# Performance work log

Hardware: AMD Instinct MI355X
Metric: run time of the kernel (lower is better)

Reference implementation:

```python
import jax, jax.numpy as jnp
import numpy as np

H = 128   # hidden_dim
M = 8     # mix_dim
N = 20000 # num_nodes
E = 320000

def gelu(x):
    return jax.nn.gelu(x, approximate=False)  # torch F.gelu default is exact erf

def setup_inputs() -> dict:
    key = jax.random.key(0)
    k1, k2, k3, k4 = jax.random.split(key, 4)
    X = jax.random.normal(k1, (N, H), dtype=jnp.float32)
    edge_index = jax.random.randint(k2, (2, E), 0, N, dtype=jnp.int64)
    # Linear weights, torch layout: y = x @ W.T
    W_A = jax.random.normal(k3, (H, H), dtype=jnp.float32) / np.sqrt(H)
    W_B = jax.random.normal(k4, (M, H), dtype=jnp.float32) / np.sqrt(H)
    return {"X": X, "edge_index": edge_index, "W_A": W_A, "W_B": W_B, "num_nodes": N}

def reference(X, edge_index, W_A, W_B, num_nodes):
    src, dst = edge_index[0], edge_index[1]
    X_src = X[src]                                   # (E, h) gather
    # compute_W_tar: W_B(gelu(W_A(X_src))), input_activation=False
    W_tar_edge = gelu(X_src @ W_A.T) @ W_B.T         # (E, m)
    # per-edge outer product, scatter_add over dst
    cross = jnp.einsum('eh,em->ehm', X_src, W_tar_edge)          # (E, h, m)
    agg = jax.ops.segment_sum(cross, dst, num_segments=num_nodes) # (N, h, m)
    agg = gelu(agg)
    # gather agg back to edges, contract over mix dim
    out_edge = jnp.einsum('ehm,em->eh', agg[dst], W_tar_edge)     # (E, h)
    # scatter_mean over dst
    ones = jnp.ones((dst.shape[0],), dtype=X.dtype)
    count = jax.ops.segment_sum(ones, dst, num_segments=num_nodes)
    out_sum = jax.ops.segment_sum(out_edge, dst, num_segments=num_nodes)
    out = out_sum / jnp.maximum(count, 1.0)[:, None]
    return out
```

## Files before the change

### kernel.cpp

```cpp
#include <hip/hip_runtime.h>
#include <hip/hip_bf16.h>


#define H 128
#define MDIM 8
#define CAP 64

typedef float v2f __attribute__((ext_vector_type(2)));

__device__ __forceinline__ float gelu_f(float x) {
    float x2 = x * x;
    float u  = x * (0.7978845608f + 0.0356774081f * x2);
    float u2 = u * u;
    float num = u * (945.0f + u2 * (105.0f + u2));
    float den = 945.0f + u2 * (420.0f + 15.0f * u2);
    float t = num * __builtin_amdgcn_rcpf(den);
    t = fminf(fmaxf(t, -1.0f), 1.0f);
    return 0.5f * (x + x * t);
}

__device__ __forceinline__ v2f gelu2(v2f x) {
    v2f x2 = x * x;
    v2f u  = x * (0.7978845608f + 0.0356774081f * x2);
    v2f u2 = u * u;
    v2f num = u * (945.0f + u2 * (105.0f + u2));
    v2f den = 945.0f + u2 * (420.0f + 15.0f * u2);
    v2f t;
    t.x = num.x * __builtin_amdgcn_rcpf(den.x);
    t.y = num.y * __builtin_amdgcn_rcpf(den.y);
    t.x = fminf(fmaxf(t.x, -1.0f), 1.0f);
    t.y = fminf(fmaxf(t.y, -1.0f), 1.0f);
    return 0.5f * (x + x * t);
}

__global__ __launch_bounds__(128) void k_prep_fill(const float* __restrict__ X,
                                                   const float* __restrict__ WA,
                                                   const float* __restrict__ WB,
                                                   const int* __restrict__ ei,
                                                   float* __restrict__ T,
                                                   int* __restrict__ cnt,
                                                   int* __restrict__ bucket,
                                                   int N, int E) {
    __shared__ float Xs[32][68];
    __shared__ float Ws[128][68];
    __shared__ float WBs[8][132];
    const int t  = threadIdx.x;
    const int n0 = blockIdx.x * 32;
    const int tn = t >> 4;
    const int tj = t & 15;

    #pragma unroll
    for (int i = 0; i < 2; ++i) {
        int idx = t + 128 * i;
        int r = idx >> 5, c4 = idx & 31;
        *(float4*)&WBs[r][c4 * 4] = *(const float4*)(WB + (size_t)r * H + c4 * 4);
    }

    float acc[4][8] = {};

    for (int kh = 0; kh < 2; ++kh) {
        __syncthreads();
        const int kb = kh * 64;
        #pragma unroll
        for (int i = 0; i < 4; ++i) {
            int idx = t + 128 * i;
            int r = idx >> 4, c4 = idx & 15;
            *(float4*)&Xs[r][c4 * 4] =
                *(const float4*)(X + (size_t)(n0 + r) * H + kb + c4 * 4);
        }
        #pragma unroll
        for (int i = 0; i < 16; ++i) {
            int idx = t + 128 * i;
            int r = idx >> 4, c4 = idx & 15;
            *(float4*)&Ws[r][c4 * 4] =
                *(const float4*)(WA + (size_t)r * H + kb + c4 * 4);
        }
        __syncthreads();

        #pragma unroll 1
        for (int k = 0; k < 64; k += 4) {
            float4 xv[4], bv[8];
            #pragma unroll
            for (int nn = 0; nn < 4; ++nn)
                xv[nn] = *(const float4*)&Xs[4 * tn + nn][k];
            #pragma unroll
            for (int jj = 0; jj < 8; ++jj)
                bv[jj] = *(const float4*)&Ws[tj + 16 * jj][k];
            #pragma unroll
            for (int nn = 0; nn < 4; ++nn)
                #pragma unroll
                for (int jj = 0; jj < 8; ++jj)
                    acc[nn][jj] += xv[nn].x * bv[jj].x + xv[nn].y * bv[jj].y +
                                   xv[nn].z * bv[jj].z + xv[nn].w * bv[jj].w;
        }
    }

    __syncthreads();
    float (*Hs)[132] = (float(*)[132])Ws;
    #pragma unroll
    for (int nn = 0; nn < 4; ++nn)
        #pragma unroll
        for (int jj = 0; jj < 8; ++jj)
            Hs[4 * tn + nn][tj + 16 * jj] = gelu_f(acc[nn][jj]);
    __syncthreads();

    #pragma unroll
    for (int i = 0; i < 2; ++i) {
        int q = t + 128 * i;
        int n = q >> 3, m = q & 7;
        float s = 0.f;
        #pragma unroll 4
        for (int kk = 0; kk < 32; ++kk) {
            float4 h = *(const float4*)&Hs[n][kk * 4];
            float4 w = *(const float4*)&WBs[m][kk * 4];
            s += h.x * w.x + h.y * w.y + h.z * w.z + h.w * w.w;
        }
        T[(size_t)(n0 + n) * MDIM + m] = s;
    }

    {
        const int stride = gridDim.x * 128;
        for (int e = blockIdx.x * 128 + t; e < E; e += stride) {
            int s  = ei[e];
            int dd = ei[E + e];
            int p  = atomicAdd(&cnt[dd], 1);
            if (p < CAP) bucket[dd * CAP + p] = s;
        }
    }
}

__device__ __forceinline__ void fma8v(v2f* acc, v2f xv, float4 ta, float4 tb) {
    acc[0] += xv * ta.x;
    acc[1] += xv * ta.y;
    acc[2] += xv * ta.z;
    acc[3] += xv * ta.w;
    acc[4] += xv * tb.x;
    acc[5] += xv * tb.y;
    acc[6] += xv * tb.z;
    acc[7] += xv * tb.w;
}

__global__ __launch_bounds__(256) void k_main(const float* __restrict__ X,
                                              const float* __restrict__ T,
                                              const int* __restrict__ cnt,
                                              const int* __restrict__ bucket,
                                              float* __restrict__ out, int N) {
    __shared__ __attribute__((aligned(16))) int srcs[4][CAP];
    __shared__ float Tl[4][CAP][MDIM];
    const int w    = threadIdx.x >> 6;
    const int lane = threadIdx.x & 63;
    const int d    = blockIdx.x * 4 + w;
    if (d >= N) return;

    const int c  = cnt[d];
    const int cc = (c < CAP) ? c : CAP;

    if (lane < cc) {
        int s = bucket[d * CAP + lane];
        srcs[w][lane] = s;
        const float4* t4 = (const float4*)(T + (size_t)s * MDIM);
        *(float4*)&Tl[w][lane][0] = t4[0];
        *(float4*)&Tl[w][lane][4] = t4[1];
    }

    float sp = 0.f;
    {
        const int m = lane & 7, g = lane >> 3;
        for (int j = g; j < cc; j += 8) sp += Tl[w][j][m];
        sp += __shfl_xor(sp, 8);
        sp += __shfl_xor(sp, 16);
        sp += __shfl_xor(sp, 32);
    }
    float S[MDIM];
    #pragma unroll
    for (int m = 0; m < MDIM; ++m) S[m] = __shfl(sp, m);

    v2f acc[MDIM] = {};
    const float* Xl = X + 2 * lane;

    int j = 0;
    for (; j + 8 <= cc; j += 8) {
        int4 sa = *(const int4*)&srcs[w][j];
        int4 sb = *(const int4*)&srcs[w][j + 4];
        v2f x0 = *(const v2f*)(Xl + (size_t)sa.x * H);
        v2f x1 = *(const v2f*)(Xl + (size_t)sa.y * H);
        v2f x2 = *(const v2f*)(Xl + (size_t)sa.z * H);
        v2f x3 = *(const v2f*)(Xl + (size_t)sa.w * H);
        v2f x4 = *(const v2f*)(Xl + (size_t)sb.x * H);
        v2f x5 = *(const v2f*)(Xl + (size_t)sb.y * H);
        v2f x6 = *(const v2f*)(Xl + (size_t)sb.z * H);
        v2f x7 = *(const v2f*)(Xl + (size_t)sb.w * H);
        #pragma unroll
        for (int q = 0; q < 8; ++q) {
            float4 ta = *(const float4*)&Tl[w][j + q][0];
            float4 tb = *(const float4*)&Tl[w][j + q][4];
            v2f xv = (q == 0) ? x0 : (q == 1) ? x1 : (q == 2) ? x2 : (q == 3) ? x3
                   : (q == 4) ? x4 : (q == 5) ? x5 : (q == 6) ? x6 : x7;
            fma8v(acc, xv, ta, tb);
        }
    }
    for (; j + 4 <= cc; j += 4) {
        int4 s4 = *(const int4*)&srcs[w][j];
        v2f x0 = *(const v2f*)(Xl + (size_t)s4.x * H);
        v2f x1 = *(const v2f*)(Xl + (size_t)s4.y * H);
        v2f x2 = *(const v2f*)(Xl + (size_t)s4.z * H);
        v2f x3 = *(const v2f*)(Xl + (size_t)s4.w * H);
        fma8v(acc, x0, *(const float4*)&Tl[w][j + 0][0], *(const float4*)&Tl[w][j + 0][4]);
        fma8v(acc, x1, *(const float4*)&Tl[w][j + 1][0], *(const float4*)&Tl[w][j + 1][4]);
        fma8v(acc, x2, *(const float4*)&Tl[w][j + 2][0], *(const float4*)&Tl[w][j + 2][4]);
        fma8v(acc, x3, *(const float4*)&Tl[w][j + 3][0], *(const float4*)&Tl[w][j + 3][4]);
    }
    for (; j < cc; ++j) {
        int s = srcs[w][j];
        v2f xv = *(const v2f*)(Xl + (size_t)s * H);
        float4 ta = *(const float4*)&Tl[w][j][0];
        float4 tb = *(const float4*)&Tl[w][j][4];
        fma8v(acc, xv, ta, tb);
    }

    v2f r = {0.f, 0.f};
    if (c > 0) {
        float inv = __builtin_amdgcn_rcpf((float)c);
        #pragma unroll
        for (int m = 0; m < MDIM; ++m) r += gelu2(acc[m]) * S[m];
        r.x *= inv;
        r.y *= inv;
    }
    *(v2f*)(out + (size_t)d * H + 2 * lane) = r;
}

extern "C" void kernel_launch(void* const* d_in, const int* in_sizes, int n_in,
                              void* d_out, int out_size, void* d_ws, size_t ws_size,
                              hipStream_t stream) {
    const float* X  = (const float*)d_in[0];
    const int*   ei = (const int*)d_in[1];
    const float* WA = (const float*)d_in[2];
    const float* WB = (const float*)d_in[3];
    float* out = (float*)d_out;

    const int N = in_sizes[0] / H;
    const int E = in_sizes[1] / 2;

    char* wp = (char*)d_ws;
    float* T    = (float*)wp;  wp += (size_t)N * MDIM * sizeof(float);
    int*   cnt  = (int*)wp;    wp += (size_t)((N + 3) & ~3) * sizeof(int);
    int*   bucket = (int*)wp;

    hipMemsetAsync(cnt, 0, (size_t)N * sizeof(int), stream);
    k_prep_fill<<<dim3(N / 32), dim3(128), 0, stream>>>(
        X, WA, WB, ei, T, cnt, bucket, N, E);
    k_main<<<dim3((N + 3) / 4), dim3(256), 0, stream>>>(X, T, cnt, bucket, out, N);
}
```

Baseline: 126.3 us.

## Compute X@W_A^T with split-bf16 MFMA and prefetch bucket sources unconditionally

```diff
diff --git a/kernel.cpp b/kernel.cpp
--- a/kernel.cpp
+++ b/kernel.cpp
@@ -1,5 +1,4 @@
 #include <hip/hip_runtime.h>
-#include <hip/hip_bf16.h>
 
 
 #define H 128
@@ -7,6 +6,11 @@
 #define CAP 64
 
 typedef float v2f __attribute__((ext_vector_type(2)));
+typedef float f32x4 __attribute__((ext_vector_type(4)));
+typedef short bf16x8 __attribute__((ext_vector_type(8)));
+typedef unsigned int uint2v __attribute__((ext_vector_type(2)));
+
+union FragCvt { unsigned int u[4]; bf16x8 s8; };
 
 __device__ __forceinline__ float gelu_f(float x) {
     float x2 = x * x;
@@ -41,67 +45,102 @@
                                                    int* __restrict__ cnt,
                                                    int* __restrict__ bucket,
                                                    int N, int E) {
-    __shared__ float Xs[32][68];
-    __shared__ float Ws[128][68];
-    __shared__ float WBs[8][132];
-    const int t  = threadIdx.x;
-    const int n0 = blockIdx.x * 32;
-    const int tn = t >> 4;
-    const int tj = t & 15;
-
+    __shared__ __align__(16) char lds[65536];
+    char* WAh = lds;
+    char* WAl = lds + 32768;
+
+    const int t    = threadIdx.x;
+    const int n0   = blockIdx.x * 32;
+    const int w    = t >> 6;
+    const int lane = t & 63;
+    const int tj   = lane & 15;
+    const int tc   = lane >> 4;
+
+    const float* xp = X + (size_t)(n0 + w * 16 + tj) * H + tc * 8;
+    f32x4 xr[8];
+    #pragma unroll
+    for (int ks = 0; ks < 4; ++ks) {
+        xr[2 * ks]     = *(const f32x4*)(xp + ks * 32);
+        xr[2 * ks + 1] = *(const f32x4*)(xp + ks * 32 + 4);
+    }
+
+    #pragma unroll
+    for (int i = 0; i < 32; ++i) {
+        int idx = t + 128 * i;
+        int r = idx >> 5, c4 = idx & 31;
+        f32x4 v = *(const f32x4*)(WA + (size_t)r * H + c4 * 4);
+        unsigned int u0 = __float_as_uint(v.x);
+        unsigned int u1 = __float_as_uint(v.y);
+        unsigned int u2 = __float_as_uint(v.z);
+        unsigned int u3 = __float_as_uint(v.w);
+        float l0 = v.x - __uint_as_float(u0 & 0xFFFF0000u);
+        float l1 = v.y - __uint_as_float(u1 & 0xFFFF0000u);
+        float l2 = v.z - __uint_as_float(u2 & 0xFFFF0000u);
+        float l3 = v.w - __uint_as_float(u3 & 0xFFFF0000u);
+        uint2v hh, ll;
+        hh.x = (u0 >> 16) | (u1 & 0xFFFF0000u);
+        hh.y = (u2 >> 16) | (u3 & 0xFFFF0000u);
+        ll.x = (__float_as_uint(l0) >> 16) | (__float_as_uint(l1) & 0xFFFF0000u);
+        ll.y = (__float_as_uint(l2) >> 16) | (__float_as_uint(l3) & 0xFFFF0000u);
+        int off = r * 256 + ((c4 * 8) ^ ((r & 7) << 4));
+        *(uint2v*)(WAh + off) = hh;
+        *(uint2v*)(WAl + off) = ll;
+    }
+    __syncthreads();
+
+    f32x4 acc[8] = {};
+    #pragma unroll
+    for (int ks = 0; ks < 4; ++ks) {
+        f32x4 a0 = xr[2 * ks], a1 = xr[2 * ks + 1];
+        unsigned int u0 = __float_as_uint(a0.x), u1 = __float_as_uint(a0.y);
+        unsigned int u2 = __float_as_uint(a0.z), u3 = __float_as_uint(a0.w);
+        unsigned int u4 = __float_as_uint(a1.x), u5 = __float_as_uint(a1.y);
+        unsigned int u6 = __float_as_uint(a1.z), u7 = __float_as_uint(a1.w);
+        FragCvt ch, cl;
+        ch.u[0] = (u0 >> 16) | (u1 & 0xFFFF0000u);
+        ch.u[1] = (u2 >> 16) | (u3 & 0xFFFF0000u);
+        ch.u[2] = (u4 >> 16) | (u5 & 0xFFFF0000u);
+        ch.u[3] = (u6 >> 16) | (u7 & 0xFFFF0000u);
+        float m0 = a0.x - __uint_as_float(u0 & 0xFFFF0000u);
+        float m1 = a0.y - __uint_as_float(u1 & 0xFFFF0000u);
+        float m2 = a0.z - __uint_as_float(u2 & 0xFFFF0000u);
+        float m3 = a0.w - __uint_as_float(u3 & 0xFFFF0000u);
+        float m4 = a1.x - __uint_as_float(u4 & 0xFFFF0000u);
+        float m5 = a1.y - __uint_as_float(u5 & 0xFFFF0000u);
+        float m6 = a1.z - __uint_as_float(u6 & 0xFFFF0000u);
+        float m7 = a1.w - __uint_as_float(u7 & 0xFFFF0000u);
+        cl.u[0] = (__float_as_uint(m0) >> 16) | (__float_as_uint(m1) & 0xFFFF0000u);
+        cl.u[1] = (__float_as_uint(m2) >> 16) | (__float_as_uint(m3) & 0xFFFF0000u);
+        cl.u[2] = (__float_as_uint(m4) >> 16) | (__float_as_uint(m5) & 0xFFFF0000u);
+        cl.u[3] = (__float_as_uint(m6) >> 16) | (__float_as_uint(m7) & 0xFFFF0000u);
+        bf16x8 ah = ch.s8, al = cl.s8;
+
+        int woff = ((ks * 64 + tc * 16) ^ ((tj & 7) << 4));
+        #pragma unroll
+        for (int ct = 0; ct < 8; ++ct) {
+            int rb = (ct * 16 + tj) * 256;
+            bf16x8 bh = *(const bf16x8*)(WAh + rb + woff);
+            bf16x8 bl = *(const bf16x8*)(WAl + rb + woff);
+            acc[ct] = __builtin_amdgcn_mfma_f32_16x16x32_bf16(ah, bh, acc[ct], 0, 0, 0);
+            acc[ct] = __builtin_amdgcn_mfma_f32_16x16x32_bf16(al, bh, acc[ct], 0, 0, 0);
+            acc[ct] = __builtin_amdgcn_mfma_f32_16x16x32_bf16(ah, bl, acc[ct], 0, 0, 0);
+        }
+    }
+    __syncthreads();
+
+    float (*Hs)[132]  = (float(*)[132])lds;
+    float (*WBs)[132] = (float(*)[132])(lds + 32768);
     #pragma unroll
     for (int i = 0; i < 2; ++i) {
         int idx = t + 128 * i;
         int r = idx >> 5, c4 = idx & 31;
-        *(float4*)&WBs[r][c4 * 4] = *(const float4*)(WB + (size_t)r * H + c4 * 4);
-    }
-
-    float acc[4][8] = {};
-
-    for (int kh = 0; kh < 2; ++kh) {
-        __syncthreads();
-        const int kb = kh * 64;
-        #pragma unroll
-        for (int i = 0; i < 4; ++i) {
-            int idx = t + 128 * i;
-            int r = idx >> 4, c4 = idx & 15;
-            *(float4*)&Xs[r][c4 * 4] =
-                *(const float4*)(X + (size_t)(n0 + r) * H + kb + c4 * 4);
-        }
-        #pragma unroll
-        for (int i = 0; i < 16; ++i) {
-            int idx = t + 128 * i;
-            int r = idx >> 4, c4 = idx & 15;
-            *(float4*)&Ws[r][c4 * 4] =
-                *(const float4*)(WA + (size_t)r * H + kb + c4 * 4);
-        }
-        __syncthreads();
-
-        #pragma unroll 1
-        for (int k = 0; k < 64; k += 4) {
-            float4 xv[4], bv[8];
-            #pragma unroll
-            for (int nn = 0; nn < 4; ++nn)
-                xv[nn] = *(const float4*)&Xs[4 * tn + nn][k];
-            #pragma unroll
-            for (int jj = 0; jj < 8; ++jj)
-                bv[jj] = *(const float4*)&Ws[tj + 16 * jj][k];
-            #pragma unroll
-            for (int nn = 0; nn < 4; ++nn)
-                #pragma unroll
-                for (int jj = 0; jj < 8; ++jj)
-                    acc[nn][jj] += xv[nn].x * bv[jj].x + xv[nn].y * bv[jj].y +
-                                   xv[nn].z * bv[jj].z + xv[nn].w * bv[jj].w;
-        }
-    }
-
-    __syncthreads();
-    float (*Hs)[132] = (float(*)[132])Ws;
-    #pragma unroll
-    for (int nn = 0; nn < 4; ++nn)
-        #pragma unroll
-        for (int jj = 0; jj < 8; ++jj)
-            Hs[4 * tn + nn][tj + 16 * jj] = gelu_f(acc[nn][jj]);
+        *(f32x4*)&WBs[r][c4 * 4] = *(const f32x4*)(WB + (size_t)r * H + c4 * 4);
+    }
+    #pragma unroll
+    for (int ct = 0; ct < 8; ++ct)
+        #pragma unroll
+        for (int q = 0; q < 4; ++q)
+            Hs[w * 16 + tc * 4 + q][ct * 16 + tj] = gelu_f(acc[ct][q]);
     __syncthreads();
 
     #pragma unroll
@@ -112,8 +151,8 @@
         #pragma unroll 4
         for (int kk = 0; kk < 32; ++kk) {
             float4 h = *(const float4*)&Hs[n][kk * 4];
-            float4 w = *(const float4*)&WBs[m][kk * 4];
-            s += h.x * w.x + h.y * w.y + h.z * w.z + h.w * w.w;
+            float4 wv = *(const float4*)&WBs[m][kk * 4];
+            s += h.x * wv.x + h.y * wv.y + h.z * wv.z + h.w * wv.w;
         }
         T[(size_t)(n0 + n) * MDIM + m] = s;
     }
@@ -152,12 +191,14 @@
     const int d    = blockIdx.x * 4 + w;
     if (d >= N) return;
 
-    const int c  = cnt[d];
-    const int cc = (c < CAP) ? c : CAP;
-
+    const int c   = cnt[d];
+    int     s_raw = bucket[d * CAP + lane];
+    const int cc  = (c < CAP) ? c : CAP;
+    int s = s_raw;
+    s = (s < 0) ? 0 : s;
+    s = (s >= N) ? 0 : s;
+    srcs[w][lane] = s;
     if (lane < cc) {
-        int s = bucket[d * CAP + lane];
-        srcs[w][lane] = s;
         const float4* t4 = (const float4*)(T + (size_t)s * MDIM);
         *(float4*)&Tl[w][lane][0] = t4[0];
         *(float4*)&Tl[w][lane][4] = t4[1];
@@ -211,8 +252,8 @@
         fma8v(acc, x3, *(const float4*)&Tl[w][j + 3][0], *(const float4*)&Tl[w][j + 3][4]);
     }
     for (; j < cc; ++j) {
-        int s = srcs[w][j];
-        v2f xv = *(const v2f*)(Xl + (size_t)s * H);
+        int ss = srcs[w][j];
+        v2f xv = *(const v2f*)(Xl + (size_t)ss * H);
         float4 ta = *(const float4*)&Tl[w][j][0];
         float4 tb = *(const float4*)&Tl[w][j][4];
         fma8v(acc, xv, ta, tb);
```

Result: no change. 128.7 us (+1.8%).
